# Kernel optimization log

Hardware: AMD Instinct MI355X
Metric: run time of the kernel (lower is better)

Reference implementation:

```python
import jax, jax.numpy as jnp
import numpy as np

N, E, B = 10000, 160000, 4096
DIN, H, C, HID, HEU = 768, 4, 256, 256, 6

def _gelu(x):
    return jax.nn.gelu(x, approximate=False)

def setup_inputs() -> dict:
    key = jax.random.key(0)
    ks = jax.random.split(key, 30)
    s = 0.02
    inp = {
        'semantic_embeddings': jax.random.normal(ks[0], (B, 2 * DIN), jnp.float32),
        'graph_x': jax.random.normal(ks[1], (N, DIN), jnp.float32),
        'graph_edge_index': jax.random.randint(ks[2], (2, E), 0, N, dtype=jnp.int32),
        'graph_edge_weight': jax.random.uniform(ks[3], (E, 1), jnp.float32),
        'heuristic_features': jax.random.uniform(ks[4], (B, HEU), jnp.float32),
        'node_indices': jax.random.randint(ks[5], (B,), 0, N, dtype=jnp.int32),
        # semantic_proj: Linear(1536,256) GELU Linear(256,256)
        'sem_w1': jax.random.normal(ks[6], (HID, 2 * DIN)) * s,
        'sem_b1': jnp.zeros((HID,), jnp.float32),
        'sem_w2': jax.random.normal(ks[7], (HID, HID)) * s,
        'sem_b2': jnp.zeros((HID,), jnp.float32),
        # GATConv(768 -> 256, heads=4, concat, edge_dim=1)
        'lin_w': jax.random.normal(ks[8], (H * C, DIN)) * s,
        'lin_edge_w': jax.random.normal(ks[9], (H * C, 1)) * s,
        'att_src': jax.random.normal(ks[10], (1, H, C)) * s,
        'att_dst': jax.random.normal(ks[11], (1, H, C)) * s,
        'att_edge': jax.random.normal(ks[12], (1, H, C)) * s,
        'gat_bias': jnp.zeros((H * C,), jnp.float32),
        # structural_proj: Linear(1024,256) GELU
        'struct_w': jax.random.normal(ks[13], (HID, H * C)) * s,
        'struct_b': jnp.zeros((HID,), jnp.float32),
        # HierarchicalResidualFusion
        'gate_w': jax.random.normal(ks[14], (HID, 2 * HID)) * s,
        'gate_b': jnp.zeros((HID,), jnp.float32),
        'heur_w': jax.random.normal(ks[15], (HID, HEU)) * s,
        'heur_b': jnp.zeros((HID,), jnp.float32),
        'hw': jnp.asarray(0.7, jnp.float32),
        'sw1': jax.random.normal(ks[16], (HID, HID)) * s,
        'sb1': jnp.zeros((HID,), jnp.float32),
        'sw2': jax.random.normal(ks[17], (1, HID)) * s,
        'sb2': jnp.zeros((1,), jnp.float32),
    }
    return inp

def reference(semantic_embeddings, graph_x, graph_edge_index, graph_edge_weight,
              heuristic_features, node_indices,
              sem_w1, sem_b1, sem_w2, sem_b2,
              lin_w, lin_edge_w, att_src, att_dst, att_edge, gat_bias,
              struct_w, struct_b,
              gate_w, gate_b, heur_w, heur_b, hw, sw1, sb1, sw2, sb2):
    # --- semantic projection (dropout = identity at eval) ---
    h = _gelu(semantic_embeddings @ sem_w1.T + sem_b1)
    h_sem = h @ sem_w2.T + sem_b2  # [B, HID]

    # --- GATConv with edge_dim=1, add_self_loops (edge_attr fill = mean) ---
    Nn = graph_x.shape[0]
    src = jnp.concatenate([graph_edge_index[0], jnp.arange(Nn, dtype=graph_edge_index.dtype)])
    dst = jnp.concatenate([graph_edge_index[1], jnp.arange(Nn, dtype=graph_edge_index.dtype)])
    ea = jnp.concatenate([graph_edge_weight,
                          jnp.broadcast_to(graph_edge_weight.mean(0, keepdims=True), (Nn, 1))], axis=0)
    x_proj = (graph_x @ lin_w.T).reshape(Nn, H, C)          # [N,H,C]
    a_src_n = (x_proj * att_src).sum(-1)                     # [N,H]
    a_dst_n = (x_proj * att_dst).sum(-1)                     # [N,H]
    e_proj = (ea @ lin_edge_w.T).reshape(-1, H, C)           # [E+N,H,C]
    alpha = a_src_n[src] + a_dst_n[dst] + (e_proj * att_edge).sum(-1)  # [E+N,H]
    alpha = jax.nn.leaky_relu(alpha, 0.2)
    amax = jax.ops.segment_max(alpha, dst, num_segments=Nn)
    expa = jnp.exp(alpha - amax[dst])
    denom = jax.ops.segment_sum(expa, dst, num_segments=Nn)
    coef = expa / denom[dst]                                 # softmax per dst node/head
    msg = x_proj[src] * coef[:, :, None]                     # [E+N,H,C]
    out = jax.ops.segment_sum(msg, dst, num_segments=Nn).reshape(Nn, H * C) + gat_bias
    h_graph = jax.nn.elu(out)

    # --- structural projection on selected nodes ---
    h_struct = _gelu(h_graph[node_indices] @ struct_w.T + struct_b)  # [B,HID]

    # --- hierarchical residual fusion ---
    h_heur = _gelu(heuristic_features @ heur_w.T + heur_b)
    g = jax.nn.sigmoid(jnp.concatenate([h_sem, h_struct], axis=-1) @ gate_w.T + gate_b)
    h_learned = g * h_sem + (1.0 - g) * h_struct
    h_fused = hw * h_heur + (1.0 - hw) * h_learned
    scores = (_gelu(h_fused @ sw1.T + sb1) @ sw2.T + sb2).squeeze(-1)  # [B]
    return scores
```

## Files before the change

### kernel.cpp

```cpp
#include <hip/hip_runtime.h>
#include <math.h>

#define DEV __device__ __forceinline__

typedef __attribute__((ext_vector_type(8))) short bf16x8;
typedef __attribute__((ext_vector_type(4))) float f32x4;

DEV float gelu_f(float x) { return 0.5f * x * (1.f + erff(x * 0.70710678118654752440f)); }

DEV unsigned short f2bf(float f) {
    unsigned u = __float_as_uint(f);
    u += 0x7FFF + ((u >> 16) & 1);
    return (unsigned short)(u >> 16);
}
DEV float bf2f(unsigned short h) { return __uint_as_float(((unsigned)h) << 16); }
DEV void split2(float v, unsigned short& h, unsigned short& l) {
    h = f2bf(v);
    l = f2bf(v - bf2f(h));
}

DEV void gload_lds16(const void* g, void* l) {
    __builtin_amdgcn_global_load_lds((const __attribute__((address_space(1))) void*)g,
                                     (__attribute__((address_space(3))) void*)l, 16, 0, 0);
}

template<int FM, int FN, int WR, int WC, int EPI, int GATHER, int ASRC, int OUT, int SPLIT>
DEV void gemm_body(char* ldsbase, int swz,
                   const unsigned short* __restrict__ Ah, const unsigned short* __restrict__ Al,
                   const float* __restrict__ Af, const int* __restrict__ gidx,
                   const unsigned short* __restrict__ Wh, const unsigned short* __restrict__ Wl,
                   const float* __restrict__ bias,
                   float* __restrict__ C, unsigned short* __restrict__ Ch, unsigned short* __restrict__ Cl,
                   int ldsp, int coff,
                   const float* __restrict__ fs_hsem, const float* __restrict__ fs_hstruct,
                   const float* __restrict__ fs_heur, const float* __restrict__ fs_heurw,
                   const float* __restrict__ fs_heurb, const float* __restrict__ fs_hw,
                   int M, int N, int K, int nbx)
{
    constexpr int BK = 64;
    constexpr int BM = WR * FM * 16, BN = WC * FN * 16;
    constexpr int NW = WR * WC;
    char* p = ldsbase;
    unsigned short* sAh = (unsigned short*)p; p += BM * BK * 2;
    unsigned short* sAl = nullptr;
    if constexpr (SPLIT) { sAl = (unsigned short*)p; p += BM * BK * 2; }
    unsigned short* sWh = (unsigned short*)p; p += BN * BK * 2;
    unsigned short* sWl = nullptr;
    if constexpr (SPLIT) { sWl = (unsigned short*)p; }

    const int tid = threadIdx.x;
    const int lane = tid & 63;
    const int wid = tid >> 6;
    const int wr = wid / WC, wc = wid % WC;

    const int bx = swz % nbx, by = swz / nbx;
    const int row0 = by * BM;
    const int col0 = bx * BN;

    f32x4 acc[FM][FN];
#pragma unroll
    for (int i = 0; i < FM; i++)
#pragma unroll
        for (int j = 0; j < FN; j++) acc[i][j] = (f32x4){0.f, 0.f, 0.f, 0.f};

    const int srow = lane >> 3;
    const int sslot = lane & 7;

    for (int k0 = 0; k0 < K; k0 += BK) {
#pragma unroll
        for (int c = 0; c < BM / 8 / NW; c++) {
            int call = c * NW + wid;
            int r = call * 8 + srow;
            int gr = row0 + r;
            gr = gr < M ? gr : M - 1;
            if (ASRC == 0) {
                if (GATHER) gr = gidx[gr];
                int b = (sslot ^ (r & 7)) << 4;
                gload_lds16((const char*)(Ah + (size_t)gr * K + k0) + b, (char*)sAh + call * 1024);
                if (SPLIT)
                    gload_lds16((const char*)(Al + (size_t)gr * K + k0) + b, (char*)sAl + call * 1024);
            } else {
                const float* sp = Af + (size_t)gr * K + k0 + sslot * 8;
                float vv[8];
                *(float4*)&vv[0] = *(const float4*)sp;
                *(float4*)&vv[4] = *(const float4*)(sp + 4);
                union { bf16x8 v; unsigned short u[8]; } ph, pl;
#pragma unroll
                for (int q = 0; q < 8; q++) split2(vv[q], ph.u[q], pl.u[q]);
                int b = (sslot ^ (r & 7)) << 4;
                *(bf16x8*)((char*)sAh + r * 128 + b) = ph.v;
                *(bf16x8*)((char*)sAl + r * 128 + b) = pl.v;
            }
        }
#pragma unroll
        for (int c = 0; c < BN / 8 / NW; c++) {
            int call = c * NW + wid;
            int r = call * 8 + srow;
            int gr = col0 + r;
            int b = (sslot ^ (r & 7)) << 4;
            gload_lds16((const char*)(Wh + (size_t)gr * K + k0) + b, (char*)sWh + call * 1024);
            if (SPLIT)
                gload_lds16((const char*)(Wl + (size_t)gr * K + k0) + b, (char*)sWl + call * 1024);
        }
        __syncthreads();

        const int fr = lane & 15, kq = lane >> 4;
#pragma unroll
        for (int ks = 0; ks < 2; ks++) {
            bf16x8 ah[FM], al[FM], bh[FN], bl[FN];
#pragma unroll
            for (int i = 0; i < FM; i++) {
                int r = wr * FM * 16 + i * 16 + fr;
                int b = ((ks * 4 + kq) ^ (r & 7)) << 4;
                ah[i] = *(const bf16x8*)((const char*)sAh + r * 128 + b);
                if (SPLIT) al[i] = *(const bf16x8*)((const char*)sAl + r * 128 + b);
            }
#pragma unroll
            for (int j = 0; j < FN; j++) {
                int r = wc * FN * 16 + j * 16 + fr;
                int b = ((ks * 4 + kq) ^ (r & 7)) << 4;
                bh[j] = *(const bf16x8*)((const char*)sWh + r * 128 + b);
                if (SPLIT) bl[j] = *(const bf16x8*)((const char*)sWl + r * 128 + b);
            }
#pragma unroll
            for (int i = 0; i < FM; i++)
#pragma unroll
                for (int j = 0; j < FN; j++) {
                    acc[i][j] = __builtin_amdgcn_mfma_f32_16x16x32_bf16(ah[i], bh[j], acc[i][j], 0, 0, 0);
                    if (SPLIT) {
                        acc[i][j] = __builtin_amdgcn_mfma_f32_16x16x32_bf16(al[i], bh[j], acc[i][j], 0, 0, 0);
                        acc[i][j] = __builtin_amdgcn_mfma_f32_16x16x32_bf16(ah[i], bl[j], acc[i][j], 0, 0, 0);
                    }
                }
        }
        __syncthreads();
    }

    const int fr = lane & 15;
    const int r0 = (lane >> 4) * 4;
#pragma unroll
    for (int i = 0; i < FM; i++) {
#pragma unroll
        for (int jj = 0; jj < 4; jj++) {
            int gr = row0 + wr * FM * 16 + i * 16 + r0 + jj;
            if (gr >= M) continue;
#pragma unroll
            for (int j = 0; j < FN; j++) {
                int gc = col0 + wc * FN * 16 + j * 16 + fr;
                float v = acc[i][j][jj] + (bias ? bias[gc] : 0.f);
                if (EPI == 1) v = gelu_f(v);
                else if (EPI == 3) {
                    float g = 1.f / (1.f + expf(-v));
                    float hh = fs_heurb[gc];
#pragma unroll
                    for (int q = 0; q < 6; q++) hh = fmaf(fs_heur[gr * 6 + q], fs_heurw[gc * 6 + q], hh);
                    hh = gelu_f(hh);
                    float hl = g * fs_hsem[(size_t)gr * 256 + gc] + (1.f - g) * fs_hstruct[(size_t)gr * 256 + gc];
                    float hwv = fs_hw[0];
                    v = hwv * hh + (1.f - hwv) * hl;
                }
                if (OUT == 0 || OUT == 2) C[(size_t)gr * N + gc] = v;
                if (OUT == 1 || OUT == 2) {
                    unsigned short h, l;
                    split2(v, h, l);
                    Ch[(size_t)gr * ldsp + coff + gc] = h;
                    Cl[(size_t)gr * ldsp + coff + gc] = l;
                }
                if (OUT == 3) Ch[(size_t)gr * ldsp + coff + gc] = f2bf(v);
            }
        }
    }
}

DEV int xcd_swz(int bid, int nwg) {
    return ((nwg & 7) == 0) ? (bid & 7) * (nwg >> 3) + (bid >> 3) : bid;
}

template<int FM, int FN, int WR, int WC, int EPI, int GATHER, int ASRC, int OUT, int SPLIT>
__global__ __launch_bounds__(WR* WC * 64)
void mgemm_k(const unsigned short* __restrict__ Ah, const unsigned short* __restrict__ Al,
             const float* __restrict__ Af, const int* __restrict__ gidx,
             const unsigned short* __restrict__ Wh, const unsigned short* __restrict__ Wl,
             const float* __restrict__ bias,
             float* __restrict__ C, unsigned short* __restrict__ Ch, unsigned short* __restrict__ Cl,
             int ldsp, int coff,
             const float* __restrict__ fs_hsem, const float* __restrict__ fs_hstruct,
             const float* __restrict__ fs_heur, const float* __restrict__ fs_heurw,
             const float* __restrict__ fs_heurb, const float* __restrict__ fs_hw,
             int M, int N, int K, int nbx)
{
    constexpr int BM = WR * FM * 16, BN = WC * FN * 16;
    constexpr int LDSB = (BM + BN) * 64 * 2 * (SPLIT ? 2 : 1);
    __shared__ alignas(16) char lds[LDSB];
    int swz = xcd_swz(blockIdx.x, gridDim.x);
    gemm_body<FM, FN, WR, WC, EPI, GATHER, ASRC, OUT, SPLIT>(
        lds, swz, Ah, Al, Af, gidx, Wh, Wl, bias, C, Ch, Cl, ldsp, coff,
        fs_hsem, fs_hstruct, fs_heur, fs_heurw, fs_heurb, fs_hw, M, N, K, nbx);
}

__global__ __launch_bounds__(256)
void dualA_k(const unsigned short* __restrict__ gxh, const unsigned short* __restrict__ linw_h,
             unsigned short* __restrict__ xpb, int Nn, int HC, int DIN, int nbx_x, int nxp,
             const float* __restrict__ sem, const unsigned short* __restrict__ sw1w_h,
             const unsigned short* __restrict__ sw1w_l, const float* __restrict__ sem_b1,
             unsigned short* __restrict__ s1h, unsigned short* __restrict__ s1l,
             int B, int nbh, int nh1)
{
    __shared__ alignas(16) char lds[32768];
    int bid = blockIdx.x;
    if (bid < nxp) {
        int swz = xcd_swz(bid, nxp);
        gemm_body<4, 4, 2, 2, 0, 0, 0, 3, 0>(
            lds, swz, gxh, nullptr, nullptr, nullptr, linw_h, nullptr, nullptr,
            nullptr, xpb, nullptr, HC, 0, nullptr, nullptr, nullptr, nullptr, nullptr, nullptr,
            Nn, HC, DIN, nbx_x);
    } else {
        int swz = xcd_swz(bid - nxp, nh1);
        gemm_body<1, 2, 2, 2, 1, 0, 1, 1, 1>(
            lds, swz, nullptr, nullptr, sem, nullptr, sw1w_h, sw1w_l, sem_b1,
            nullptr, s1h, s1l, 256, 0, nullptr, nullptr, nullptr, nullptr, nullptr, nullptr,
            B, 256, 2 * DIN, nbh);
    }
}

__global__ __launch_bounds__(256)
void dualB_k(const unsigned short* __restrict__ s1h, const unsigned short* __restrict__ s1l,
             const unsigned short* __restrict__ sw2w_h, const unsigned short* __restrict__ sw2w_l,
             const float* __restrict__ sem_b2, float* __restrict__ h_sem,
             const unsigned short* __restrict__ aggh, const unsigned short* __restrict__ aggl,
             const int* __restrict__ nidx,
             const unsigned short* __restrict__ stw_h, const unsigned short* __restrict__ stw_l,
             const float* __restrict__ struct_b, float* __restrict__ h_struct,
             unsigned short* __restrict__ gAh, unsigned short* __restrict__ gAl,
             int B, int HC, int nbh, int nsem)
{
    __shared__ alignas(16) char lds[24576];
    int bid = blockIdx.x;
    if (bid < nsem) {
        int swz = xcd_swz(bid, nsem);
        gemm_body<1, 2, 2, 2, 0, 0, 0, 2, 1>(
            lds, swz, s1h, s1l, nullptr, nullptr, sw2w_h, sw2w_l, sem_b2,
            h_sem, gAh, gAl, 512, 0, nullptr, nullptr, nullptr, nullptr, nullptr, nullptr,
            B, 256, 256, nbh);
    } else {
        int swz = xcd_swz(bid - nsem, nsem);
        gemm_body<1, 2, 2, 2, 1, 1, 0, 2, 1>(
            lds, swz, aggh, aggl, nullptr, nidx, stw_h, stw_l, struct_b,
            h_struct, gAh, gAl, 512, 256, nullptr, nullptr, nullptr, nullptr, nullptr, nullptr,
            B, 256, HC, nbh);
    }
}


__global__ void init_k(int* count, int* needed, float* scal, int Nn,
                       const float* __restrict__ lin_w, const float* __restrict__ att_src,
                       const float* __restrict__ att_dst,
                       float* __restrict__ wsrc, float* __restrict__ wdst,
                       const float* __restrict__ lew, const float* __restrict__ ae, int ZB)
{
    int b = blockIdx.x;
    if (b < ZB) {
        int i = b * 256 + threadIdx.x;
        if (i < Nn) { count[i] = 0; needed[i] = 0; }
        if (i == 0) scal[0] = 0.f;
        return;
    }
    if (b < ZB + 12) {
        int gid = (b - ZB) * 256 + threadIdx.x;
        if (gid >= 4 * 768) return;
        int h = gid / 768, k = gid % 768;
        float ss = 0.f, sd = 0.f;
        for (int c = 0; c < 256; c++) {
            float w = lin_w[(size_t)(h * 256 + c) * 768 + k];
            ss = fmaf(w, att_src[h * 256 + c], ss);
            sd = fmaf(w, att_dst[h * 256 + c], sd);
        }
        wsrc[k * 4 + h] = ss;
        wdst[k * 4 + h] = sd;
        return;
    }
    int w = threadIdx.x / 64, lane = threadIdx.x % 64;
    float c = 0.f;
    for (int cc = lane; cc < 256; cc += 64) c += lew[w * 256 + cc] * ae[w * 256 + cc];
    for (int off = 32; off; off >>= 1) c += __shfl_down(c, off);
    if (lane == 0) scal[1 + w] = c;
}

__global__ __launch_bounds__(256)
void mega1_k(int Nn, int nW, int nCnt, int nMark, int nEw,
             const float* __restrict__ gx, unsigned short* __restrict__ gxh,
             const float* __restrict__ wsrc, const float* __restrict__ wdst,
             float* __restrict__ a_src, float* __restrict__ a_dst,
             const float* s0, unsigned short* h0, unsigned short* l0, int e0,
             const float* s1, unsigned short* h1, unsigned short* l1, int e1,
             const float* s2, unsigned short* h2, unsigned short* l2, int e2,
             const float* s3, unsigned short* h3, unsigned short* l3, int e3,
             const float* s4, unsigned short* h4, unsigned short* l4, int e4,
             const float* s5, unsigned short* h5, unsigned short* l5, int e5,
             const int* __restrict__ ei, int* __restrict__ count, int E,
             const int* __restrict__ nidx, int* __restrict__ needed, int B,
             const float* __restrict__ ew, float* __restrict__ scal)
{
    __shared__ float sh[256];
    int b = blockIdx.x;
    int t = threadIdx.x;

    if (b < Nn) {
        int node = b;
        float acc[8] = {0.f, 0.f, 0.f, 0.f, 0.f, 0.f, 0.f, 0.f};
        if (t < 192) {
            float4 v = ((const float4*)(gx + (size_t)node * 768))[t];
            ushort4 h;
            h.x = f2bf(v.x); h.y = f2bf(v.y); h.z = f2bf(v.z); h.w = f2bf(v.w);
            ((ushort4*)(gxh + (size_t)node * 768))[t] = h;
            float vv[4] = {v.x, v.y, v.z, v.w};
#pragma unroll
            for (int q = 0; q < 4; q++) {
                int k = t * 4 + q;
                float4 wsv = *(const float4*)(wsrc + k * 4);
                float4 wdv = *(const float4*)(wdst + k * 4);
                acc[0] = fmaf(vv[q], wsv.x, acc[0]); acc[1] = fmaf(vv[q], wsv.y, acc[1]);
                acc[2] = fmaf(vv[q], wsv.z, acc[2]); acc[3] = fmaf(vv[q], wsv.w, acc[3]);
                acc[4] = fmaf(vv[q], wdv.x, acc[4]); acc[5] = fmaf(vv[q], wdv.y, acc[5]);
                acc[6] = fmaf(vv[q], wdv.z, acc[6]); acc[7] = fmaf(vv[q], wdv.w, acc[7]);
            }
        }
#pragma unroll
        for (int i = 0; i < 8; i++)
            for (int off = 32; off; off >>= 1) acc[i] += __shfl_down(acc[i], off);
        int lane = t & 63, wid = t >> 6;
        if (lane == 0)
#pragma unroll
            for (int i = 0; i < 8; i++) sh[wid * 8 + i] = acc[i];
        __syncthreads();
        if (t < 8) {
            float s = sh[t] + sh[8 + t] + sh[16 + t] + sh[24 + t];
            if (t < 4) a_src[node * 4 + t] = s;
            else       a_dst[node * 4 + (t - 4)] = s;
        }
        return;
    }
    b -= Nn;
    if (b < nW) {
        int i = b * 256 + t;
        const float* s; unsigned short* h; unsigned short* l; int j;
        if (i < e0)      { s = s0; h = h0; l = l0; j = i; }
        else if (i < e1) { s = s1; h = h1; l = l1; j = i - e0; }
        else if (i < e2) { s = s2; h = h2; l = l2; j = i - e1; }
        else if (i < e3) { s = s3; h = h3; l = l3; j = i - e2; }
        else if (i < e4) { s = s4; h = h4; l = l4; j = i - e3; }
        else if (i < e5) { s = s5; h = h5; l = l5; j = i - e4; }
        else return;
        float4 v = ((const float4*)s)[j];
        ushort4 hh, ll;
        split2(v.x, hh.x, ll.x);
        split2(v.y, hh.y, ll.y);
        split2(v.z, hh.z, ll.z);
        split2(v.w, hh.w, ll.w);
        ((ushort4*)h)[j] = hh;
        ((ushort4*)l)[j] = ll;
        return;
    }
    b -= nW;
    if (b < nCnt) {
        int e = b * 256 + t;
        if (e >= E + Nn) return;
        int d = (e < E) ? ei[E + e] : e - E;
        atomicAdd(&count[d], 1);
        return;
    }
    b -= nCnt;
    if (b < nMark) {
        int gid = b * 256 + t;
        if (gid < B) needed[nidx[gid]] = 1;
        return;
    }
    b -= nMark;
    float s = 0.f;
    for (int i = b * 256 + t; i < E; i += nEw * 256) s += ew[i];
    sh[t] = s;
    __syncthreads();
    for (int off = 128; off; off >>= 1) {
        if (t < off) sh[t] += sh[t + off];
        __syncthreads();
    }
    if (t == 0) atomicAdd(&scal[0], sh[0]);
}

__global__ __launch_bounds__(1024) void scan_k(const int* __restrict__ count, int* __restrict__ offs, int Nn)
{
    __shared__ int sums[1024];
    int t = threadIdx.x;
    int C = (Nn + 1023) >> 10;
    int lo = t * C, hi = min(lo + C, Nn);
    int s = 0;
    for (int i = lo; i < hi; i++) s += count[i];
    sums[t] = s;
    __syncthreads();
    for (int off = 1; off < 1024; off <<= 1) {
        int add = (t >= off) ? sums[t - off] : 0;
        __syncthreads();
        sums[t] += add;
        __syncthreads();
    }
    int run = t ? sums[t - 1] : 0;
    for (int i = lo; i < hi; i++) { offs[i] = run; run += count[i]; }
}

__global__ void fill_k(const int* __restrict__ ei, int* __restrict__ offs,
                       int* __restrict__ eid, int E, int Nn)
{
    int e = blockIdx.x * 256 + threadIdx.x;
    if (e >= E + Nn) return;
    int d = (e < E) ? ei[E + e] : e - E;
    int p = atomicAdd(&offs[d], 1);
    eid[p] = e;
}

#define CHK 256
__global__ __launch_bounds__(256)
void gat_agg_k(const int* __restrict__ ei, const float* __restrict__ ew,
               const float* __restrict__ scal, const float* __restrict__ a_src,
               const float* __restrict__ a_dst, const int* __restrict__ needed,
               const int* __restrict__ count, const int* __restrict__ offs_end,
               const int* __restrict__ eid, const unsigned short* __restrict__ xpb,
               const float* __restrict__ gat_bias,
               unsigned short* __restrict__ aggh, unsigned short* __restrict__ aggl,
               int E, int Nn)
{
    int d = blockIdx.x;
    if (!needed[d]) return;
    int c = count[d];
    int start = offs_end[d] - c;
    int tid = threadIdx.x;
    __shared__ int   srcs[CHK];
    __shared__ float al[CHK * 4];
    __shared__ float mrun[4], drun[4], scale[4];
    if (tid < 4) { mrun[tid] = -1e30f; drun[tid] = 0.f; }
    float4 acc = make_float4(0.f, 0.f, 0.f, 0.f);
    const int h = tid >> 6;
    const int x = tid * 4;
    const float adst0 = a_dst[d * 4 + 0], adst1 = a_dst[d * 4 + 1],
                adst2 = a_dst[d * 4 + 2], adst3 = a_dst[d * 4 + 3];

    for (int cb = 0; cb < c; cb += CHK) {
        int cc = min(CHK, c - cb);
        __syncthreads();
        for (int t = tid; t < cc * 4; t += 256) {
            int j = t >> 2, hh = t & 3;
            int e = eid[start + cb + j];
            int s; float ea;
            if (e < E) { s = ei[e]; ea = ew[e]; }
            else       { s = e - E; ea = scal[0] / (float)E; }
            float ad = hh == 0 ? adst0 : hh == 1 ? adst1 : hh == 2 ? adst2 : adst3;
            float a = a_src[s * 4 + hh] + ad + ea * scal[1 + hh];
            a = a > 0.f ? a : 0.2f * a;
            al[j * 4 + hh] = a;
            if (hh == 0) srcs[j] = s;
        }
        __syncthreads();
        if (tid < 4) {
            float m = -1e30f;
            for (int j = 0; j < cc; j++) m = fmaxf(m, al[j * 4 + tid]);
            float nm = fmaxf(mrun[tid], m);
            float sc = expf(mrun[tid] - nm);
            scale[tid] = sc;
            drun[tid] *= sc;
            mrun[tid] = nm;
        }
        __syncthreads();
        for (int t = tid; t < cc * 4; t += 256) {
            int j = t >> 2, hh = t & 3;
            al[j * 4 + hh] = expf(al[j * 4 + hh] - mrun[hh]);
        }
        __syncthreads();
        if (tid < 4) {
            float s = 0.f;
            for (int j = 0; j < cc; j++) s += al[j * 4 + tid];
            drun[tid] += s;
        }
        float sc = scale[h];
        acc.x *= sc; acc.y *= sc; acc.z *= sc; acc.w *= sc;
        for (int j = 0; j < cc; j++) {
            float w = al[j * 4 + h];
            ushort4 vv = *(const ushort4*)(xpb + (size_t)srcs[j] * 1024 + x);
            acc.x = fmaf(w, bf2f(vv.x), acc.x);
            acc.y = fmaf(w, bf2f(vv.y), acc.y);
            acc.z = fmaf(w, bf2f(vv.z), acc.z);
            acc.w = fmaf(w, bf2f(vv.w), acc.w);
        }
    }
    __syncthreads();
    float dn = drun[h];
    float4 gb = *(const float4*)(gat_bias + x);
    float t0 = acc.x / dn + gb.x, t1 = acc.y / dn + gb.y,
          t2 = acc.z / dn + gb.z, t3 = acc.w / dn + gb.w;
    t0 = t0 > 0.f ? t0 : expf(t0) - 1.f;
    t1 = t1 > 0.f ? t1 : expf(t1) - 1.f;
    t2 = t2 > 0.f ? t2 : expf(t2) - 1.f;
    t3 = t3 > 0.f ? t3 : expf(t3) - 1.f;
    ushort4 hh, ll;
    split2(t0, hh.x, ll.x);
    split2(t1, hh.y, ll.y);
    split2(t2, hh.z, ll.z);
    split2(t3, hh.w, ll.w);
    *(ushort4*)(aggh + (size_t)d * 1024 + x) = hh;
    *(ushort4*)(aggl + (size_t)d * 1024 + x) = ll;
}

__global__ void score_k(const float* __restrict__ s1, const float* __restrict__ sw2,
                        const float* __restrict__ sb2, float* __restrict__ out, int B)
{
    int b = blockIdx.x * 4 + threadIdx.x / 64;
    int lane = threadIdx.x % 64;
    if (b >= B) return;
    float4 v = *(const float4*)(s1 + (size_t)b * 256 + lane * 4);
    float4 w = *(const float4*)(sw2 + lane * 4);
    float s = v.x * w.x + v.y * w.y + v.z * w.z + v.w * w.w;
    for (int off = 32; off; off >>= 1) s += __shfl_down(s, off);
    if (lane == 0) out[b] = s + sb2[0];
}


extern "C" void kernel_launch(void* const* d_in, const int* in_sizes, int n_in,
                              void* d_out, int out_size, void* d_ws, size_t ws_size,
                              hipStream_t stream)
{
    const float* sem      = (const float*)d_in[0];
    const float* gx       = (const float*)d_in[1];
    const int*   ei       = (const int*)d_in[2];
    const float* ew       = (const float*)d_in[3];
    const float* heur     = (const float*)d_in[4];
    const int*   nidx     = (const int*)d_in[5];
    const float* sem_w1   = (const float*)d_in[6];
    const float* sem_b1   = (const float*)d_in[7];
    const float* sem_w2   = (const float*)d_in[8];
    const float* sem_b2   = (const float*)d_in[9];
    const float* lin_w    = (const float*)d_in[10];
    const float* lin_edge = (const float*)d_in[11];
    const float* att_src  = (const float*)d_in[12];
    const float* att_dst  = (const float*)d_in[13];
    const float* att_edge = (const float*)d_in[14];
    const float* gat_bias = (const float*)d_in[15];
    const float* struct_w = (const float*)d_in[16];
    const float* struct_b = (const float*)d_in[17];
    const float* gate_w   = (const float*)d_in[18];
    const float* gate_b   = (const float*)d_in[19];
    const float* heur_w   = (const float*)d_in[20];
    const float* heur_b   = (const float*)d_in[21];
    const float* hwp      = (const float*)d_in[22];
    const float* sw1      = (const float*)d_in[23];
    const float* sb1      = (const float*)d_in[24];
    const float* sw2      = (const float*)d_in[25];
    const float* sb2      = (const float*)d_in[26];
    float* out = (float*)d_out;

    const int DIN = 768, HC = 1024, HID = 256;
    const int B  = in_sizes[0] / (2 * DIN);
    const int Nn = in_sizes[1] / DIN;
    const int E  = in_sizes[3];

    float* ws = (float*)d_ws;
    size_t off = 0;
    auto alloc = [&](size_t n) { float* p = ws + off; off += n; return p; };
    auto allocU = [&](size_t nelem) { return (unsigned short*)alloc((nelem + 1) / 2); };

    unsigned short* xpb  = allocU((size_t)Nn * HC);
    unsigned short* aggh = allocU((size_t)Nn * HC);
    unsigned short* aggl = allocU((size_t)Nn * HC);
    float* h_sem    = alloc((size_t)B * HID);
    float* h_struct = alloc((size_t)B * HID);
    float* s1f      = alloc((size_t)B * HID);
    unsigned short* s1h = allocU((size_t)B * HID);
    unsigned short* s1l = allocU((size_t)B * HID);
    unsigned short* gAh = allocU((size_t)B * 512);
    unsigned short* gAl = allocU((size_t)B * 512);
    unsigned short* fuh = allocU((size_t)B * HID);
    unsigned short* ful = allocU((size_t)B * HID);
    float* a_src    = alloc((size_t)Nn * 4);
    float* a_dst    = alloc((size_t)Nn * 4);
    float* wsrc     = alloc((size_t)DIN * 4);
    float* wdst     = alloc((size_t)DIN * 4);
    int* countb     = (int*)alloc((size_t)Nn);
    int* offsb      = (int*)alloc((size_t)Nn);
    int* neededb    = (int*)alloc((size_t)Nn);
    int* eidb       = (int*)alloc((size_t)(E + Nn));
    float* scal     = alloc(8);
    unsigned short* linw_h = allocU((size_t)HC * DIN);
    unsigned short* linw_l = allocU((size_t)HC * DIN);
    unsigned short* sw1w_h = allocU((size_t)HID * 2 * DIN);
    unsigned short* sw1w_l = allocU((size_t)HID * 2 * DIN);
    unsigned short* sw2w_h = allocU((size_t)HID * HID);
    unsigned short* sw2w_l = allocU((size_t)HID * HID);
    unsigned short* stw_h  = allocU((size_t)HID * HC);
    unsigned short* stw_l  = allocU((size_t)HID * HC);
    unsigned short* gaw_h  = allocU((size_t)HID * 512);
    unsigned short* gaw_l  = allocU((size_t)HID * 512);
    unsigned short* scw_h  = allocU((size_t)HID * HID);
    unsigned short* scw_l  = allocU((size_t)HID * HID);
    unsigned short* gxh    = allocU((size_t)Nn * DIN);
    (void)ws_size; (void)n_in; (void)out_size;

    int ZB = (Nn + 255) / 256;
    init_k<<<ZB + 13, 256, 0, stream>>>(countb, neededb, scal, Nn,
                                        lin_w, att_src, att_dst, wsrc, wdst,
                                        lin_edge, att_edge, ZB);

    int c0 = (HC * DIN) / 4;
    int c1 = c0 + (HID * 2 * DIN) / 4;
    int c2 = c1 + (HID * HID) / 4;
    int c3 = c2 + (HID * HC) / 4;
    int c4 = c3 + (HID * 512) / 4;
    int c5 = c4 + (HID * HID) / 4;
    int nW = (c5 + 255) / 256;
    int tot = E + Nn;
    int nCnt = (tot + 255) / 256;
    int nMark = (B + 255) / 256;
    int nEw = 256;
    mega1_k<<<Nn + nW + nCnt + nMark + nEw, 256, 0, stream>>>(
        Nn, nW, nCnt, nMark, nEw,
        gx, gxh, wsrc, wdst, a_src, a_dst,
        lin_w, linw_h, linw_l, c0,
        sem_w1, sw1w_h, sw1w_l, c1,
        sem_w2, sw2w_h, sw2w_l, c2,
        struct_w, stw_h, stw_l, c3,
        gate_w, gaw_h, gaw_l, c4,
        sw1, scw_h, scw_l, c5,
        ei, countb, E,
        nidx, neededb, B,
        ew, scal);

    scan_k<<<1, 1024, 0, stream>>>(countb, offsb, Nn);
    fill_k<<<(tot + 255) / 256, 256, 0, stream>>>(ei, offsb, eidb, E, Nn);

    const int nbx_x = HC / 128;
    const int nby_x = (Nn + 127) / 128;
    const int nxp = nbx_x * nby_x;
    const int nbh = HID / 64;
    const int nh1 = (B / 32) * nbh;
    dualA_k<<<nxp + nh1, 256, 0, stream>>>(gxh, linw_h, xpb, Nn, HC, DIN, nbx_x, nxp,
                                           sem, sw1w_h, sw1w_l, sem_b1, s1h, s1l, B, nbh, nh1);

    gat_agg_k<<<Nn, 256, 0, stream>>>(ei, ew, scal, a_src, a_dst, neededb, countb, offsb, eidb,
                                      xpb, gat_bias, aggh, aggl, E, Nn);

    dualB_k<<<2 * nh1, 256, 0, stream>>>(s1h, s1l, sw2w_h, sw2w_l, sem_b2, h_sem,
                                         aggh, aggl, nidx, stw_h, stw_l, struct_b, h_struct,
                                         gAh, gAl, B, HC, nbh, nh1);

    mgemm_k<1, 2, 2, 2, 3, 0, 0, 1, 1><<<nh1, 256, 0, stream>>>(
        gAh, gAl, nullptr, nullptr, gaw_h, gaw_l, gate_b,
        nullptr, fuh, ful, HID, 0, h_sem, h_struct, heur, heur_w, heur_b, hwp,
        B, HID, 512, nbh);

    mgemm_k<1, 2, 2, 2, 1, 0, 0, 0, 1><<<nh1, 256, 0, stream>>>(
        fuh, ful, nullptr, nullptr, scw_h, scw_l, sb1,
        s1f, nullptr, nullptr, 0, 0, nullptr, nullptr, nullptr, nullptr, nullptr, nullptr,
        B, HID, HID, nbh);

    score_k<<<B / 4, 256, 0, stream>>>(s1f, sw2, sb2, out, B);
}
```

Measured before the change: 211.4 us.

## Merge CSR build, GAT aggregation and final score into fewer fused launches

Replaces the single-block scan with an atomic cursor allocator and folds the edge-fill pass into the xproj/semantic GEMM launch. The GAT aggregation and the second semantic GEMM now share one launch, and the structural GEMM moves to its own kernel afterwards. The final score dot product is fused into the last GEMM epilogue through shuffle reductions and atomicAdd into an output pre-initialised with the bias. These changes cut launches and the serial scan cost, but the fill blocks now run concurrently with the xproj GEMM, and the atomic score accumulation makes the summation order nondeterministic.

```diff
diff --git a/kernel.cpp b/kernel.cpp
--- a/kernel.cpp
+++ b/kernel.cpp
@@ -144,6 +144,7 @@
         for (int jj = 0; jj < 4; jj++) {
             int gr = row0 + wr * FM * 16 + i * 16 + r0 + jj;
             if (gr >= M) continue;
+            float sacc = 0.f;
 #pragma unroll
             for (int j = 0; j < FN; j++) {
                 int gc = col0 + wc * FN * 16 + j * 16 + fr;
@@ -167,6 +168,14 @@
                     Cl[(size_t)gr * ldsp + coff + gc] = l;
                 }
                 if (OUT == 3) Ch[(size_t)gr * ldsp + coff + gc] = f2bf(v);
+                if (OUT == 4) sacc = fmaf(v, fs_hsem[gc], sacc);
+            }
+            if (OUT == 4) {
+                sacc += __shfl_xor(sacc, 1);
+                sacc += __shfl_xor(sacc, 2);
+                sacc += __shfl_xor(sacc, 4);
+                sacc += __shfl_xor(sacc, 8);
+                if ((lane & 15) == 0) atomicAdd(&C[gr], sacc);
             }
         }
     }
@@ -198,13 +207,103 @@
         fs_hsem, fs_hstruct, fs_heur, fs_heurw, fs_heurb, fs_hw, M, N, K, nbx);
 }
 
+DEV void gat_agg_body(char* shm, int d,
+                      const int* __restrict__ ei, const float* __restrict__ ew,
+                      const float* __restrict__ scal, const float* __restrict__ a_src,
+                      const float* __restrict__ a_dst,
+                      const int* __restrict__ count, const int* __restrict__ offs_end,
+                      const int* __restrict__ eid, const unsigned short* __restrict__ xpb,
+                      const float* __restrict__ gat_bias,
+                      unsigned short* __restrict__ aggh, unsigned short* __restrict__ aggl, int E)
+{
+    int* srcs   = (int*)shm;
+    float* al   = (float*)(shm + 1024);
+    float* mrun = (float*)(shm + 5120);
+    float* drun = (float*)(shm + 5136);
+    float* scale = (float*)(shm + 5152);
+    int c = count[d];
+    int start = offs_end[d] - c;
+    int tid = threadIdx.x;
+    if (tid < 4) { mrun[tid] = -1e30f; drun[tid] = 0.f; }
+    float4 acc = make_float4(0.f, 0.f, 0.f, 0.f);
+    const int h = tid >> 6;
+    const int x = tid * 4;
+    const float adst0 = a_dst[d * 4 + 0], adst1 = a_dst[d * 4 + 1],
+                adst2 = a_dst[d * 4 + 2], adst3 = a_dst[d * 4 + 3];
+
+    for (int cb = 0; cb < c; cb += 256) {
+        int cc = min(256, c - cb);
+        __syncthreads();
+        for (int t = tid; t < cc * 4; t += 256) {
+            int j = t >> 2, hh = t & 3;
+            int e = eid[start + cb + j];
+            int s; float ea;
+            if (e < E) { s = ei[e]; ea = ew[e]; }
+            else       { s = e - E; ea = scal[0] / (float)E; }
+            float ad = hh == 0 ? adst0 : hh == 1 ? adst1 : hh == 2 ? adst2 : adst3;
+            float a = a_src[s * 4 + hh] + ad + ea * scal[1 + hh];
+            a = a > 0.f ? a : 0.2f * a;
+            al[j * 4 + hh] = a;
+            if (hh == 0) srcs[j] = s;
+        }
+        __syncthreads();
+        if (tid < 4) {
+            float m = -1e30f;
+            for (int j = 0; j < cc; j++) m = fmaxf(m, al[j * 4 + tid]);
+            float nm = fmaxf(mrun[tid], m);
+            float sc = expf(mrun[tid] - nm);
+            scale[tid] = sc;
+            drun[tid] *= sc;
+            mrun[tid] = nm;
+        }
+        __syncthreads();
+        for (int t = tid; t < cc * 4; t += 256) {
+            int j = t >> 2, hh = t & 3;
+            al[j * 4 + hh] = expf(al[j * 4 + hh] - mrun[hh]);
+        }
+        __syncthreads();
+        if (tid < 4) {
+            float s = 0.f;
+            for (int j = 0; j < cc; j++) s += al[j * 4 + tid];
+            drun[tid] += s;
+        }
+        float sc = scale[h];
+        acc.x *= sc; acc.y *= sc; acc.z *= sc; acc.w *= sc;
+        for (int j = 0; j < cc; j++) {
+            float w = al[j * 4 + h];
+            ushort4 vv = *(const ushort4*)(xpb + (size_t)srcs[j] * 1024 + x);
+            acc.x = fmaf(w, bf2f(vv.x), acc.x);
+            acc.y = fmaf(w, bf2f(vv.y), acc.y);
+            acc.z = fmaf(w, bf2f(vv.z), acc.z);
+            acc.w = fmaf(w, bf2f(vv.w), acc.w);
+        }
+    }
+    __syncthreads();
+    float dn = drun[h];
+    float4 gb = *(const float4*)(gat_bias + x);
+    float t0 = acc.x / dn + gb.x, t1 = acc.y / dn + gb.y,
+          t2 = acc.z / dn + gb.z, t3 = acc.w / dn + gb.w;
+    t0 = t0 > 0.f ? t0 : expf(t0) - 1.f;
+    t1 = t1 > 0.f ? t1 : expf(t1) - 1.f;
+    t2 = t2 > 0.f ? t2 : expf(t2) - 1.f;
+    t3 = t3 > 0.f ? t3 : expf(t3) - 1.f;
+    ushort4 hh, ll;
+    split2(t0, hh.x, ll.x);
+    split2(t1, hh.y, ll.y);
+    split2(t2, hh.z, ll.z);
+    split2(t3, hh.w, ll.w);
+    *(ushort4*)(aggh + (size_t)d * 1024 + x) = hh;
+    *(ushort4*)(aggl + (size_t)d * 1024 + x) = ll;
+}
+
 __global__ __launch_bounds__(256)
 void dualA_k(const unsigned short* __restrict__ gxh, const unsigned short* __restrict__ linw_h,
              unsigned short* __restrict__ xpb, int Nn, int HC, int DIN, int nbx_x, int nxp,
              const float* __restrict__ sem, const unsigned short* __restrict__ sw1w_h,
              const unsigned short* __restrict__ sw1w_l, const float* __restrict__ sem_b1,
              unsigned short* __restrict__ s1h, unsigned short* __restrict__ s1l,
-             int B, int nbh, int nh1)
+             int B, int nbh, int nh1,
+             const int* __restrict__ ei, int* __restrict__ offs, int* __restrict__ eid, int E)
 {
     __shared__ alignas(16) char lds[32768];
     int bid = blockIdx.x;
@@ -214,40 +313,49 @@
             lds, swz, gxh, nullptr, nullptr, nullptr, linw_h, nullptr, nullptr,
             nullptr, xpb, nullptr, HC, 0, nullptr, nullptr, nullptr, nullptr, nullptr, nullptr,
             Nn, HC, DIN, nbx_x);
-    } else {
+    } else if (bid < nxp + nh1) {
         int swz = xcd_swz(bid - nxp, nh1);
         gemm_body<1, 2, 2, 2, 1, 0, 1, 1, 1>(
             lds, swz, nullptr, nullptr, sem, nullptr, sw1w_h, sw1w_l, sem_b1,
             nullptr, s1h, s1l, 256, 0, nullptr, nullptr, nullptr, nullptr, nullptr, nullptr,
             B, 256, 2 * DIN, nbh);
+    } else {
+        int e = (bid - nxp - nh1) * 256 + threadIdx.x;
+        if (e < E + Nn) {
+            int d = (e < E) ? ei[E + e] : e - E;
+            int p = atomicAdd(&offs[d], 1);
+            eid[p] = e;
+        }
     }
 }
 
 __global__ __launch_bounds__(256)
-void dualB_k(const unsigned short* __restrict__ s1h, const unsigned short* __restrict__ s1l,
+void dualC_k(int Nn, int nh1,
+             const int* __restrict__ ei, const float* __restrict__ ew,
+             const float* __restrict__ scal, const float* __restrict__ a_src,
+             const float* __restrict__ a_dst, const int* __restrict__ needed,
+             const int* __restrict__ count, const int* __restrict__ offs_end,
+             const int* __restrict__ eid, const unsigned short* __restrict__ xpb,
+             const float* __restrict__ gat_bias,
+             unsigned short* __restrict__ aggh, unsigned short* __restrict__ aggl, int E,
+             const unsigned short* __restrict__ s1h, const unsigned short* __restrict__ s1l,
              const unsigned short* __restrict__ sw2w_h, const unsigned short* __restrict__ sw2w_l,
              const float* __restrict__ sem_b2, float* __restrict__ h_sem,
-             const unsigned short* __restrict__ aggh, const unsigned short* __restrict__ aggl,
-             const int* __restrict__ nidx,
-             const unsigned short* __restrict__ stw_h, const unsigned short* __restrict__ stw_l,
-             const float* __restrict__ struct_b, float* __restrict__ h_struct,
              unsigned short* __restrict__ gAh, unsigned short* __restrict__ gAl,
-             int B, int HC, int nbh, int nsem)
+             int B, int nbh)
 {
     __shared__ alignas(16) char lds[24576];
     int bid = blockIdx.x;
-    if (bid < nsem) {
-        int swz = xcd_swz(bid, nsem);
+    if (bid < Nn) {
+        if (!needed[bid]) return;
+        gat_agg_body(lds, bid, ei, ew, scal, a_src, a_dst, count, offs_end, eid,
+                     xpb, gat_bias, aggh, aggl, E);
+    } else {
+        int swz = xcd_swz(bid - Nn, nh1);
         gemm_body<1, 2, 2, 2, 0, 0, 0, 2, 1>(
             lds, swz, s1h, s1l, nullptr, nullptr, sw2w_h, sw2w_l, sem_b2,
             h_sem, gAh, gAl, 512, 0, nullptr, nullptr, nullptr, nullptr, nullptr, nullptr,
             B, 256, 256, nbh);
-    } else {
-        int swz = xcd_swz(bid - nsem, nsem);
-        gemm_body<1, 2, 2, 2, 1, 1, 0, 2, 1>(
-            lds, swz, aggh, aggl, nullptr, nidx, stw_h, stw_l, struct_b,
-            h_struct, gAh, gAl, 512, 256, nullptr, nullptr, nullptr, nullptr, nullptr, nullptr,
-            B, 256, HC, nbh);
     }
 }
 
@@ -256,13 +364,16 @@
                        const float* __restrict__ lin_w, const float* __restrict__ att_src,
                        const float* __restrict__ att_dst,
                        float* __restrict__ wsrc, float* __restrict__ wdst,
-                       const float* __restrict__ lew, const float* __restrict__ ae, int ZB)
+                       const float* __restrict__ lew, const float* __restrict__ ae, int ZB,
+                       float* __restrict__ out, const float* __restrict__ sb2, int B,
+                       int* __restrict__ cursor)
 {
     int b = blockIdx.x;
     if (b < ZB) {
         int i = b * 256 + threadIdx.x;
         if (i < Nn) { count[i] = 0; needed[i] = 0; }
-        if (i == 0) scal[0] = 0.f;
+        if (i < B) out[i] = sb2[0];
+        if (i == 0) { scal[0] = 0.f; cursor[0] = 0; }
         return;
     }
     if (b < ZB + 12) {
@@ -387,138 +498,11 @@
     if (t == 0) atomicAdd(&scal[0], sh[0]);
 }
 
-__global__ __launch_bounds__(1024) void scan_k(const int* __restrict__ count, int* __restrict__ offs, int Nn)
-{
-    __shared__ int sums[1024];
-    int t = threadIdx.x;
-    int C = (Nn + 1023) >> 10;
-    int lo = t * C, hi = min(lo + C, Nn);
-    int s = 0;
-    for (int i = lo; i < hi; i++) s += count[i];
-    sums[t] = s;
-    __syncthreads();
-    for (int off = 1; off < 1024; off <<= 1) {
-        int add = (t >= off) ? sums[t - off] : 0;
-        __syncthreads();
-        sums[t] += add;
-        __syncthreads();
-    }
-    int run = t ? sums[t - 1] : 0;
-    for (int i = lo; i < hi; i++) { offs[i] = run; run += count[i]; }
-}
-
-__global__ void fill_k(const int* __restrict__ ei, int* __restrict__ offs,
-                       int* __restrict__ eid, int E, int Nn)
-{
-    int e = blockIdx.x * 256 + threadIdx.x;
-    if (e >= E + Nn) return;
-    int d = (e < E) ? ei[E + e] : e - E;
-    int p = atomicAdd(&offs[d], 1);
-    eid[p] = e;
-}
-
-#define CHK 256
-__global__ __launch_bounds__(256)
-void gat_agg_k(const int* __restrict__ ei, const float* __restrict__ ew,
-               const float* __restrict__ scal, const float* __restrict__ a_src,
-               const float* __restrict__ a_dst, const int* __restrict__ needed,
-               const int* __restrict__ count, const int* __restrict__ offs_end,
-               const int* __restrict__ eid, const unsigned short* __restrict__ xpb,
-               const float* __restrict__ gat_bias,
-               unsigned short* __restrict__ aggh, unsigned short* __restrict__ aggl,
-               int E, int Nn)
-{
-    int d = blockIdx.x;
-    if (!needed[d]) return;
-    int c = count[d];
-    int start = offs_end[d] - c;
-    int tid = threadIdx.x;
-    __shared__ int   srcs[CHK];
-    __shared__ float al[CHK * 4];
-    __shared__ float mrun[4], drun[4], scale[4];
-    if (tid < 4) { mrun[tid] = -1e30f; drun[tid] = 0.f; }
-    float4 acc = make_float4(0.f, 0.f, 0.f, 0.f);
-    const int h = tid >> 6;
-    const int x = tid * 4;
-    const float adst0 = a_dst[d * 4 + 0], adst1 = a_dst[d * 4 + 1],
-                adst2 = a_dst[d * 4 + 2], adst3 = a_dst[d * 4 + 3];
-
-    for (int cb = 0; cb < c; cb += CHK) {
-        int cc = min(CHK, c - cb);
-        __syncthreads();
-        for (int t = tid; t < cc * 4; t += 256) {
-            int j = t >> 2, hh = t & 3;
-            int e = eid[start + cb + j];
-            int s; float ea;
-            if (e < E) { s = ei[e]; ea = ew[e]; }
-            else       { s = e - E; ea = scal[0] / (float)E; }
-            float ad = hh == 0 ? adst0 : hh == 1 ? adst1 : hh == 2 ? adst2 : adst3;
-            float a = a_src[s * 4 + hh] + ad + ea * scal[1 + hh];
-            a = a > 0.f ? a : 0.2f * a;
-            al[j * 4 + hh] = a;
-            if (hh == 0) srcs[j] = s;
-        }
-        __syncthreads();
-        if (tid < 4) {
-            float m = -1e30f;
-            for (int j = 0; j < cc; j++) m = fmaxf(m, al[j * 4 + tid]);
-            float nm = fmaxf(mrun[tid], m);
-            float sc = expf(mrun[tid] - nm);
-            scale[tid] = sc;
-            drun[tid] *= sc;
-            mrun[tid] = nm;
-        }
-        __syncthreads();
-        for (int t = tid; t < cc * 4; t += 256) {
-            int j = t >> 2, hh = t & 3;
-            al[j * 4 + hh] = expf(al[j * 4 + hh] - mrun[hh]);
-        }
-        __syncthreads();
-        if (tid < 4) {
-            float s = 0.f;
-            for (int j = 0; j < cc; j++) s += al[j * 4 + tid];
-            drun[tid] += s;
-        }
-        float sc = scale[h];
-        acc.x *= sc; acc.y *= sc; acc.z *= sc; acc.w *= sc;
-        for (int j = 0; j < cc; j++) {
-            float w = al[j * 4 + h];
-            ushort4 vv = *(const ushort4*)(xpb + (size_t)srcs[j] * 1024 + x);
-            acc.x = fmaf(w, bf2f(vv.x), acc.x);
-            acc.y = fmaf(w, bf2f(vv.y), acc.y);
-            acc.z = fmaf(w, bf2f(vv.z), acc.z);
-            acc.w = fmaf(w, bf2f(vv.w), acc.w);
-        }
-    }
-    __syncthreads();
-    float dn = drun[h];
-    float4 gb = *(const float4*)(gat_bias + x);
-    float t0 = acc.x / dn + gb.x, t1 = acc.y / dn + gb.y,
-          t2 = acc.z / dn + gb.z, t3 = acc.w / dn + gb.w;
-    t0 = t0 > 0.f ? t0 : expf(t0) - 1.f;
-    t1 = t1 > 0.f ? t1 : expf(t1) - 1.f;
-    t2 = t2 > 0.f ? t2 : expf(t2) - 1.f;
-    t3 = t3 > 0.f ? t3 : expf(t3) - 1.f;
-    ushort4 hh, ll;
-    split2(t0, hh.x, ll.x);
-    split2(t1, hh.y, ll.y);
-    split2(t2, hh.z, ll.z);
-    split2(t3, hh.w, ll.w);
-    *(ushort4*)(aggh + (size_t)d * 1024 + x) = hh;
-    *(ushort4*)(aggl + (size_t)d * 1024 + x) = ll;
-}
-
-__global__ void score_k(const float* __restrict__ s1, const float* __restrict__ sw2,
-                        const float* __restrict__ sb2, float* __restrict__ out, int B)
-{
-    int b = blockIdx.x * 4 + threadIdx.x / 64;
-    int lane = threadIdx.x % 64;
-    if (b >= B) return;
-    float4 v = *(const float4*)(s1 + (size_t)b * 256 + lane * 4);
-    float4 w = *(const float4*)(sw2 + lane * 4);
-    float s = v.x * w.x + v.y * w.y + v.z * w.z + v.w * w.w;
-    for (int off = 32; off; off >>= 1) s += __shfl_down(s, off);
-    if (lane == 0) out[b] = s + sb2[0];
+__global__ void alloc_k(const int* __restrict__ count, int* __restrict__ offs,
+                        int* __restrict__ cursor, int Nn)
+{
+    int d = blockIdx.x * 256 + threadIdx.x;
+    if (d < Nn) offs[d] = atomicAdd(cursor, count[d]);
 }
 
 
@@ -570,7 +554,6 @@
     unsigned short* aggl = allocU((size_t)Nn * HC);
     float* h_sem    = alloc((size_t)B * HID);
     float* h_struct = alloc((size_t)B * HID);
-    float* s1f      = alloc((size_t)B * HID);
     unsigned short* s1h = allocU((size_t)B * HID);
     unsigned short* s1l = allocU((size_t)B * HID);
     unsigned short* gAh = allocU((size_t)B * 512);
@@ -586,6 +569,7 @@
     int* neededb    = (int*)alloc((size_t)Nn);
     int* eidb       = (int*)alloc((size_t)(E + Nn));
     float* scal     = alloc(8);
+    int* cursorb    = (int*)alloc(4);
     unsigned short* linw_h = allocU((size_t)HC * DIN);
     unsigned short* linw_l = allocU((size_t)HC * DIN);
     unsigned short* sw1w_h = allocU((size_t)HID * 2 * DIN);
@@ -604,7 +588,7 @@
     int ZB = (Nn + 255) / 256;
     init_k<<<ZB + 13, 256, 0, stream>>>(countb, neededb, scal, Nn,
                                         lin_w, att_src, att_dst, wsrc, wdst,
-                                        lin_edge, att_edge, ZB);
+                                        lin_edge, att_edge, ZB, out, sb2, B, cursorb);
 
     int c0 = (HC * DIN) / 4;
     int c1 = c0 + (HID * 2 * DIN) / 4;
@@ -630,33 +614,36 @@
         nidx, neededb, B,
         ew, scal);
 
-    scan_k<<<1, 1024, 0, stream>>>(countb, offsb, Nn);
-    fill_k<<<(tot + 255) / 256, 256, 0, stream>>>(ei, offsb, eidb, E, Nn);
+    alloc_k<<<(Nn + 255) / 256, 256, 0, stream>>>(countb, offsb, cursorb, Nn);
 
     const int nbx_x = HC / 128;
     const int nby_x = (Nn + 127) / 128;
     const int nxp = nbx_x * nby_x;
     const int nbh = HID / 64;
     const int nh1 = (B / 32) * nbh;
-    dualA_k<<<nxp + nh1, 256, 0, stream>>>(gxh, linw_h, xpb, Nn, HC, DIN, nbx_x, nxp,
-                                           sem, sw1w_h, sw1w_l, sem_b1, s1h, s1l, B, nbh, nh1);
-
-    gat_agg_k<<<Nn, 256, 0, stream>>>(ei, ew, scal, a_src, a_dst, neededb, countb, offsb, eidb,
-                                      xpb, gat_bias, aggh, aggl, E, Nn);
-
-    dualB_k<<<2 * nh1, 256, 0, stream>>>(s1h, s1l, sw2w_h, sw2w_l, sem_b2, h_sem,
-                                         aggh, aggl, nidx, stw_h, stw_l, struct_b, h_struct,
-                                         gAh, gAl, B, HC, nbh, nh1);
+    const int nF = (tot + 255) / 256;
+    dualA_k<<<nxp + nh1 + nF, 256, 0, stream>>>(gxh, linw_h, xpb, Nn, HC, DIN, nbx_x, nxp,
+                                                sem, sw1w_h, sw1w_l, sem_b1, s1h, s1l,
+                                                B, nbh, nh1, ei, offsb, eidb, E);
+
+    dualC_k<<<Nn + nh1, 256, 0, stream>>>(Nn, nh1,
+                                          ei, ew, scal, a_src, a_dst, neededb, countb, offsb, eidb,
+                                          xpb, gat_bias, aggh, aggl, E,
+                                          s1h, s1l, sw2w_h, sw2w_l, sem_b2, h_sem,
+                                          gAh, gAl, B, nbh);
+
+    mgemm_k<1, 2, 2, 2, 1, 1, 0, 2, 1><<<nh1, 256, 0, stream>>>(
+        aggh, aggl, nullptr, nidx, stw_h, stw_l, struct_b,
+        h_struct, gAh, gAl, 512, 256, nullptr, nullptr, nullptr, nullptr, nullptr, nullptr,
+        B, HID, HC, nbh);
 
     mgemm_k<1, 2, 2, 2, 3, 0, 0, 1, 1><<<nh1, 256, 0, stream>>>(
         gAh, gAl, nullptr, nullptr, gaw_h, gaw_l, gate_b,
         nullptr, fuh, ful, HID, 0, h_sem, h_struct, heur, heur_w, heur_b, hwp,
         B, HID, 512, nbh);
 
-    mgemm_k<1, 2, 2, 2, 1, 0, 0, 0, 1><<<nh1, 256, 0, stream>>>(
+    mgemm_k<1, 2, 2, 2, 1, 0, 0, 4, 1><<<nh1, 256, 0, stream>>>(
         fuh, ful, nullptr, nullptr, scw_h, scw_l, sb1,
-        s1f, nullptr, nullptr, 0, 0, nullptr, nullptr, nullptr, nullptr, nullptr, nullptr,
+        out, nullptr, nullptr, 0, 0, sw2, nullptr, nullptr, nullptr, nullptr, nullptr,
         B, HID, HID, nbh);
-
-    score_k<<<B / 4, 256, 0, stream>>>(s1f, sw2, sb2, out, B);
-}
+}
```

Measured after the change: 199.8 us. 5.5% less time.
